# Performance work log

Measured on AMD Instinct MI355X. Metric: run time of the kernel, lower is better.

Reference implementation:

```python
import jax, jax.numpy as jnp
import numpy as np

B, L, D = 64, 4096, 1024
FILL = -10000.0  # sentinel used by the original masked_fill before the sort


def setup_inputs() -> dict:
    key = jax.random.key(0)
    k1, k2 = jax.random.split(key)
    features = jax.random.normal(k1, (B, L, D), dtype=jnp.float32)
    lengths = jax.random.randint(k2, (B,), 0, L, dtype=jnp.int32)
    return {"features": features, "lengths": lengths}


def reference(features, lengths):
    # Original: mask invalid positions with -10000, sort descending along seq,
    # zero out masked slots, take element 0. Mathematically this is a masked
    # max over valid positions (and 0 if a sequence has length 0, since the
    # second masked_fill zeroes position 0 when mask[:,0] is False).
    L_ = features.shape[1]
    mask = jnp.arange(L_)[None, :] < lengths[:, None]            # [B, L]
    masked = jnp.where(mask[:, :, None], features, FILL)          # [B, L, D]
    pooled = jnp.max(masked, axis=1)                              # [B, D]
    pooled = jnp.where((lengths > 0)[:, None], pooled, 0.0)
    pool_weights = None
    return pooled
```

## Files before the change

### kernel.cpp

```cpp
#include <hip/hip_runtime.h>

#define FILLV (-10000.0f)

typedef __attribute__((ext_vector_type(4))) float f32x4;

__device__ __forceinline__ f32x4 vmax4(f32x4 a, f32x4 b) {
    f32x4 r;
    r.x = fmaxf(a.x, b.x);
    r.y = fmaxf(a.y, b.y);
    r.z = fmaxf(a.z, b.z);
    r.w = fmaxf(a.w, b.w);
    return r;
}

__device__ __forceinline__ f32x4 ntload(const f32x4* p) {
    return __builtin_nontemporal_load(p);
}

__device__ __forceinline__ f32x4 fillv4() {
    f32x4 v = {FILLV, FILLV, FILLV, FILLV};
    return v;
}

__global__ void feasel_partial_kernel(const float* __restrict__ feat,
                                      const int* __restrict__ lengths,
                                      float* __restrict__ part,
                                      int L, int DV, int segLen) {
    const int b = blockIdx.x;
    const int s = blockIdx.y;
    const int S = gridDim.y;
    const int t = threadIdx.x;

    const int len = lengths[b];
    const int l0 = s * segLen;
    const int l1 = min(min(l0 + segLen, len), L);

    const f32x4* __restrict__ p =
        reinterpret_cast<const f32x4*>(feat) + (size_t)b * L * DV + (size_t)l0 * DV + t;

    f32x4 a0 = fillv4(), a1 = fillv4(), a2 = fillv4(), a3 = fillv4();
    f32x4 a4 = fillv4(), a5 = fillv4(), a6 = fillv4(), a7 = fillv4();

    int l = l0;
    for (; l + 8 <= l1; l += 8) {
        f32x4 v0 = ntload(p + 0 * (size_t)DV);
        f32x4 v1 = ntload(p + 1 * (size_t)DV);
        f32x4 v2 = ntload(p + 2 * (size_t)DV);
        f32x4 v3 = ntload(p + 3 * (size_t)DV);
        f32x4 v4 = ntload(p + 4 * (size_t)DV);
        f32x4 v5 = ntload(p + 5 * (size_t)DV);
        f32x4 v6 = ntload(p + 6 * (size_t)DV);
        f32x4 v7 = ntload(p + 7 * (size_t)DV);
        a0 = vmax4(a0, v0);
        a1 = vmax4(a1, v1);
        a2 = vmax4(a2, v2);
        a3 = vmax4(a3, v3);
        a4 = vmax4(a4, v4);
        a5 = vmax4(a5, v5);
        a6 = vmax4(a6, v6);
        a7 = vmax4(a7, v7);
        p += 8 * (size_t)DV;
    }
    for (; l < l1; ++l) {
        a0 = vmax4(a0, ntload(p));
        p += DV;
    }

    a0 = vmax4(a0, a1);
    a2 = vmax4(a2, a3);
    a4 = vmax4(a4, a5);
    a6 = vmax4(a6, a7);
    a0 = vmax4(vmax4(a0, a2), vmax4(a4, a6));

    reinterpret_cast<f32x4*>(part)[((size_t)b * S + s) * DV + t] = a0;
}

__global__ void feasel_reduce_kernel(const float* __restrict__ part,
                                     const int* __restrict__ lengths,
                                     float* __restrict__ out,
                                     int DV, int S) {
    const int b = blockIdx.x;
    const int c = blockIdx.y * 64 + threadIdx.x;
    if (c >= DV) return;

    const f32x4* __restrict__ p =
        reinterpret_cast<const f32x4*>(part) + (size_t)b * S * DV + c;

    f32x4 a0 = fillv4(), a1 = fillv4(), a2 = fillv4(), a3 = fillv4();
    int s = 0;
    for (; s + 4 <= S; s += 4) {
        a0 = vmax4(a0, p[(size_t)(s + 0) * DV]);
        a1 = vmax4(a1, p[(size_t)(s + 1) * DV]);
        a2 = vmax4(a2, p[(size_t)(s + 2) * DV]);
        a3 = vmax4(a3, p[(size_t)(s + 3) * DV]);
    }
    for (; s < S; ++s)
        a0 = vmax4(a0, p[(size_t)s * DV]);
    a0 = vmax4(vmax4(a0, a1), vmax4(a2, a3));

    if (lengths[b] <= 0) {
        f32x4 z = {0.f, 0.f, 0.f, 0.f};
        a0 = z;
    }
    reinterpret_cast<f32x4*>(out)[(size_t)b * DV + c] = a0;
}

__global__ void feasel_direct_kernel(const float* __restrict__ feat,
                                     const int* __restrict__ lengths,
                                     float* __restrict__ out,
                                     int L, int DV) {
    const int b = blockIdx.x;
    const int t = threadIdx.x;
    const int len = min(lengths[b], L);

    const f32x4* __restrict__ p =
        reinterpret_cast<const f32x4*>(feat) + (size_t)b * L * DV + t;

    f32x4 a0 = fillv4(), a1 = fillv4(), a2 = fillv4(), a3 = fillv4();
    int l = 0;
    for (; l + 4 <= len; l += 4) {
        a0 = vmax4(a0, ntload(p + 0 * (size_t)DV));
        a1 = vmax4(a1, ntload(p + 1 * (size_t)DV));
        a2 = vmax4(a2, ntload(p + 2 * (size_t)DV));
        a3 = vmax4(a3, ntload(p + 3 * (size_t)DV));
        p += 4 * (size_t)DV;
    }
    for (; l < len; ++l) {
        a0 = vmax4(a0, ntload(p));
        p += DV;
    }
    a0 = vmax4(vmax4(a0, a1), vmax4(a2, a3));
    if (len <= 0) {
        f32x4 z = {0.f, 0.f, 0.f, 0.f};
        a0 = z;
    }
    reinterpret_cast<f32x4*>(out)[(size_t)b * DV + t] = a0;
}

extern "C" void kernel_launch(void* const* d_in, const int* in_sizes, int n_in,
                              void* d_out, int out_size, void* d_ws, size_t ws_size,
                              hipStream_t stream) {
    const float* feat    = (const float*)d_in[0];
    const int*   lengths = (const int*)d_in[1];
    float*       out     = (float*)d_out;

    const int B  = in_sizes[1];
    const int D  = out_size / B;
    const int DV = D / 4;
    const int L  = in_sizes[0] / (B * D);

    int S = 64;
    while (S > 1 && (size_t)B * S * D * sizeof(float) > ws_size) S >>= 1;

    if ((size_t)B * S * D * sizeof(float) <= ws_size) {
        float* part = (float*)d_ws;
        const int segLen = (L + S - 1) / S;
        dim3 grid1(B, S);
        feasel_partial_kernel<<<grid1, DV, 0, stream>>>(feat, lengths, part, L, DV, segLen);
        dim3 grid2(B, (DV + 63) / 64);
        feasel_reduce_kernel<<<grid2, 64, 0, stream>>>(part, lengths, out, DV, S);
    } else {
        feasel_direct_kernel<<<B, DV, 0, stream>>>(feat, lengths, out, L, DV);
    }
}
```

Baseline: 116.3 us.

## Compact work list of valid segments with persistent grid-stride blocks

The partial kernel now builds a prefix sum in shared memory of the segments that hold valid positions per batch. A fixed grid of 1024 blocks walks that compacted work list, finding each item's batch by binary search, so no blocks are launched for fully masked segments. The segment count goes up to 128 and the reduce kernel only reads the valid partials. This is meant to remove idle or empty blocks and balance load across uneven lengths, at the cost of a per-block prefix-sum prologue and hardcoding blockDim to 256, which assumes DV equals 256.

```diff
diff --git a/kernel.cpp b/kernel.cpp
--- a/kernel.cpp
+++ b/kernel.cpp
@@ -22,87 +22,107 @@
     return v;
 }
 
-__global__ void feasel_partial_kernel(const float* __restrict__ feat,
-                                      const int* __restrict__ lengths,
-                                      float* __restrict__ part,
-                                      int L, int DV, int segLen) {
-    const int b = blockIdx.x;
-    const int s = blockIdx.y;
-    const int S = gridDim.y;
+__global__ __launch_bounds__(256, 4)
+void feasel_partial_kernel(const float* __restrict__ feat,
+                           const int* __restrict__ lengths,
+                           float* __restrict__ part,
+                           int B, int L, int DV, int seg, int S) {
+    __shared__ int off[1025];
     const int t = threadIdx.x;
 
-    const int len = lengths[b];
-    const int l0 = s * segLen;
-    const int l1 = min(min(l0 + segLen, len), L);
+    for (int b = t; b < B; b += blockDim.x) {
+        int len = lengths[b];
+        len = len < 0 ? 0 : (len > L ? L : len);
+        int n = (len + seg - 1) / seg;
+        if (n > S) n = S;
+        off[b + 1] = n;
+    }
+    __syncthreads();
+    if (t == 0) {
+        off[0] = 0;
+        for (int b = 0; b < B; ++b) off[b + 1] += off[b];
+    }
+    __syncthreads();
+    const int W = off[B];
 
-    const f32x4* __restrict__ p =
-        reinterpret_cast<const f32x4*>(feat) + (size_t)b * L * DV + (size_t)l0 * DV + t;
+    for (int i = blockIdx.x; i < W; i += gridDim.x) {
+        int lo = 0, hi = B;
+        while (hi - lo > 1) {
+            int m = (lo + hi) >> 1;
+            if (off[m] <= i) lo = m; else hi = m;
+        }
+        const int b = lo;
+        const int s = i - off[lo];
 
-    f32x4 a0 = fillv4(), a1 = fillv4(), a2 = fillv4(), a3 = fillv4();
-    f32x4 a4 = fillv4(), a5 = fillv4(), a6 = fillv4(), a7 = fillv4();
+        int len = lengths[b];
+        len = len > L ? L : len;
+        const int l0 = s * seg;
+        const int l1 = min(l0 + seg, len);
 
-    int l = l0;
-    for (; l + 8 <= l1; l += 8) {
-        f32x4 v0 = ntload(p + 0 * (size_t)DV);
-        f32x4 v1 = ntload(p + 1 * (size_t)DV);
-        f32x4 v2 = ntload(p + 2 * (size_t)DV);
-        f32x4 v3 = ntload(p + 3 * (size_t)DV);
-        f32x4 v4 = ntload(p + 4 * (size_t)DV);
-        f32x4 v5 = ntload(p + 5 * (size_t)DV);
-        f32x4 v6 = ntload(p + 6 * (size_t)DV);
-        f32x4 v7 = ntload(p + 7 * (size_t)DV);
-        a0 = vmax4(a0, v0);
-        a1 = vmax4(a1, v1);
-        a2 = vmax4(a2, v2);
-        a3 = vmax4(a3, v3);
-        a4 = vmax4(a4, v4);
-        a5 = vmax4(a5, v5);
-        a6 = vmax4(a6, v6);
-        a7 = vmax4(a7, v7);
-        p += 8 * (size_t)DV;
+        const f32x4* __restrict__ p =
+            reinterpret_cast<const f32x4*>(feat) + (size_t)b * L * DV + (size_t)l0 * DV + t;
+
+        f32x4 a0 = fillv4(), a1 = fillv4(), a2 = fillv4(), a3 = fillv4();
+
+        int l = l0;
+        for (; l + 8 <= l1; l += 8) {
+            f32x4 v0 = ntload(p + 0 * (size_t)DV);
+            f32x4 v1 = ntload(p + 1 * (size_t)DV);
+            f32x4 v2 = ntload(p + 2 * (size_t)DV);
+            f32x4 v3 = ntload(p + 3 * (size_t)DV);
+            f32x4 v4 = ntload(p + 4 * (size_t)DV);
+            f32x4 v5 = ntload(p + 5 * (size_t)DV);
+            f32x4 v6 = ntload(p + 6 * (size_t)DV);
+            f32x4 v7 = ntload(p + 7 * (size_t)DV);
+            a0 = vmax4(a0, vmax4(v0, v4));
+            a1 = vmax4(a1, vmax4(v1, v5));
+            a2 = vmax4(a2, vmax4(v2, v6));
+            a3 = vmax4(a3, vmax4(v3, v7));
+            p += 8 * (size_t)DV;
+        }
+        for (; l < l1; ++l) {
+            a0 = vmax4(a0, ntload(p));
+            p += DV;
+        }
+        a0 = vmax4(vmax4(a0, a1), vmax4(a2, a3));
+
+        reinterpret_cast<f32x4*>(part)[((size_t)b * S + s) * DV + t] = a0;
     }
-    for (; l < l1; ++l) {
-        a0 = vmax4(a0, ntload(p));
-        p += DV;
-    }
-
-    a0 = vmax4(a0, a1);
-    a2 = vmax4(a2, a3);
-    a4 = vmax4(a4, a5);
-    a6 = vmax4(a6, a7);
-    a0 = vmax4(vmax4(a0, a2), vmax4(a4, a6));
-
-    reinterpret_cast<f32x4*>(part)[((size_t)b * S + s) * DV + t] = a0;
 }
 
 __global__ void feasel_reduce_kernel(const float* __restrict__ part,
                                      const int* __restrict__ lengths,
                                      float* __restrict__ out,
-                                     int DV, int S) {
+                                     int L, int DV, int seg, int S) {
     const int b = blockIdx.x;
     const int c = blockIdx.y * 64 + threadIdx.x;
     if (c >= DV) return;
 
-    const f32x4* __restrict__ p =
-        reinterpret_cast<const f32x4*>(part) + (size_t)b * S * DV + c;
+    int len = lengths[b];
+    len = len < 0 ? 0 : (len > L ? L : len);
+    int nseg = (len + seg - 1) / seg;
+    if (nseg > S) nseg = S;
 
-    f32x4 a0 = fillv4(), a1 = fillv4(), a2 = fillv4(), a3 = fillv4();
-    int s = 0;
-    for (; s + 4 <= S; s += 4) {
-        a0 = vmax4(a0, p[(size_t)(s + 0) * DV]);
-        a1 = vmax4(a1, p[(size_t)(s + 1) * DV]);
-        a2 = vmax4(a2, p[(size_t)(s + 2) * DV]);
-        a3 = vmax4(a3, p[(size_t)(s + 3) * DV]);
+    f32x4 acc;
+    if (len <= 0) {
+        f32x4 z = {0.f, 0.f, 0.f, 0.f};
+        acc = z;
+    } else {
+        const f32x4* __restrict__ p =
+            reinterpret_cast<const f32x4*>(part) + (size_t)b * S * DV + c;
+        f32x4 a0 = fillv4(), a1 = fillv4(), a2 = fillv4(), a3 = fillv4();
+        int s = 0;
+        for (; s + 4 <= nseg; s += 4) {
+            a0 = vmax4(a0, p[(size_t)(s + 0) * DV]);
+            a1 = vmax4(a1, p[(size_t)(s + 1) * DV]);
+            a2 = vmax4(a2, p[(size_t)(s + 2) * DV]);
+            a3 = vmax4(a3, p[(size_t)(s + 3) * DV]);
+        }
+        for (; s < nseg; ++s)
+            a0 = vmax4(a0, p[(size_t)s * DV]);
+        acc = vmax4(vmax4(a0, a1), vmax4(a2, a3));
     }
-    for (; s < S; ++s)
-        a0 = vmax4(a0, p[(size_t)s * DV]);
-    a0 = vmax4(vmax4(a0, a1), vmax4(a2, a3));
-
-    if (lengths[b] <= 0) {
-        f32x4 z = {0.f, 0.f, 0.f, 0.f};
-        a0 = z;
-    }
-    reinterpret_cast<f32x4*>(out)[(size_t)b * DV + c] = a0;
+    reinterpret_cast<f32x4*>(out)[(size_t)b * DV + c] = acc;
 }
 
 __global__ void feasel_direct_kernel(const float* __restrict__ feat,
@@ -111,7 +131,8 @@
                                      int L, int DV) {
     const int b = blockIdx.x;
     const int t = threadIdx.x;
-    const int len = min(lengths[b], L);
+    int len = lengths[b];
+    len = len < 0 ? 0 : (len > L ? L : len);
 
     const f32x4* __restrict__ p =
         reinterpret_cast<const f32x4*>(feat) + (size_t)b * L * DV + t;
@@ -149,16 +170,18 @@
     const int DV = D / 4;
     const int L  = in_sizes[0] / (B * D);
 
-    int S = 64;
+    int S = 128;
     while (S > 1 && (size_t)B * S * D * sizeof(float) > ws_size) S >>= 1;
 
-    if ((size_t)B * S * D * sizeof(float) <= ws_size) {
-        float* part = (float*)d_ws;
-        const int segLen = (L + S - 1) / S;
-        dim3 grid1(B, S);
-        feasel_partial_kernel<<<grid1, DV, 0, stream>>>(feat, lengths, part, L, DV, segLen);
+    if ((size_t)B * S * D * sizeof(float) <= ws_size && B <= 1024) {
+        float* part   = (float*)d_ws;
+        const int seg = (L + S - 1) / S;
+
+        feasel_partial_kernel<<<1024, 256, 0, stream>>>(feat, lengths, part,
+                                                        B, L, DV, seg, S);
+
         dim3 grid2(B, (DV + 63) / 64);
-        feasel_reduce_kernel<<<grid2, 64, 0, stream>>>(part, lengths, out, DV, S);
+        feasel_reduce_kernel<<<grid2, 64, 0, stream>>>(part, lengths, out, L, DV, seg, S);
     } else {
         feasel_direct_kernel<<<B, DV, 0, stream>>>(feat, lengths, out, L, DV);
     }
```

New measurement: 105.5 us. -9.3%, faster.
